# Kernel optimization log

Hardware: AMD Instinct MI355X
Metric: run time of the kernel (lower is better)

## Reference

```python
import jax, jax.numpy as jnp
import numpy as np

R = 2  # decimation factor


def _cheby1_sos(N=8, rp=0.05, Wn=1.0 / R):
    """Chebyshev type-I lowpass, second-order sections (matches scipy.signal.cheby1 math)."""
    eps = np.sqrt(10.0 ** (rp / 10.0) - 1.0)
    mu = np.arcsinh(1.0 / eps) / N
    k = np.arange(1, N + 1)
    theta = np.pi * (2 * k - 1) / (2 * N)
    # analog prototype poles (no zeros)
    p = -np.sinh(mu) * np.sin(theta) + 1j * np.cosh(mu) * np.cos(theta)
    gain = np.real(np.prod(-p))
    if N % 2 == 0:
        gain /= np.sqrt(1.0 + eps * eps)
    # prewarp + lp2lp
    fs = 2.0
    warped = 2.0 * fs * np.tan(np.pi * Wn / fs)
    p = p * warped
    gain = gain * warped ** N
    # bilinear transform (zeros -> z=-1, order N)
    fs2 = 2.0 * fs
    pz = (fs2 + p) / (fs2 - p)
    gain = gain / np.real(np.prod(fs2 - p))
    # pair complex-conjugate poles into biquads (N even, all complex)
    pp = pz[np.imag(pz) > 0]
    a1 = -2.0 * np.real(pp)
    a2 = np.abs(pp) ** 2
    g = gain ** (1.0 / len(pp))  # distribute gain evenly across sections
    b0 = np.full(len(pp), g)
    sos = np.stack([b0, 2.0 * b0, b0, np.ones(len(pp)), a1, a2], axis=1)
    return sos  # [nsec, 6] float64


_SOS = _cheby1_sos()


def _sosfilt(x):
    """Cascaded biquads, direct form II transposed, zero initial state. x: [B, T]."""
    B = x.shape[0]
    nsec = _SOS.shape[0]
    b0 = jnp.asarray(_SOS[:, 0], x.dtype)
    b1 = jnp.asarray(_SOS[:, 1], x.dtype)
    b2 = jnp.asarray(_SOS[:, 2], x.dtype)
    a1 = jnp.asarray(_SOS[:, 4], x.dtype)
    a2 = jnp.asarray(_SOS[:, 5], x.dtype)

    def step(carry, xt):  # carry: (z1, z2) each [B, nsec]; xt: [B]
        z1, z2 = carry
        y = xt
        nz1, nz2 = [], []
        for s in range(nsec):  # fixed small unroll over sections
            out = b0[s] * y + z1[:, s]
            nz1.append(b1[s] * y + z2[:, s] - a1[s] * out)
            nz2.append(b2[s] * y - a2[s] * out)
            y = out
        return (jnp.stack(nz1, axis=1), jnp.stack(nz2, axis=1)), y

    z0 = jnp.zeros((B, nsec), x.dtype)
    _, ys = jax.lax.scan(step, (z0, z0), x.T)  # scan over time
    return ys.T  # [B, T]


def setup_inputs() -> dict:
    key = jax.random.key(0)
    x = jax.random.normal(key, (32, 131072), dtype=jnp.float32)
    return {"x": x}


def reference(x) -> jnp.ndarray:
    y = _sosfilt(x)
    return y[..., ::R]
```

## Files before the change

### kernel.cpp

```cpp
#include <hip/hip_runtime.h>
#include <cmath>
#include <complex>


#define T_LEN   131072
#define B_ROWS  32
#define OUT_LEN (T_LEN / 2)
#define L_CHUNK 64
#define H_WARM  192
#define TPB     256
#define BLOCKS_PER_ROW (T_LEN / (L_CHUNK * TPB))
#define WIN_FLOATS (TPB * L_CHUNK + H_WARM)
#define WIN_UNITS  (WIN_FLOATS / 4)
#define NBLOCKS (B_ROWS * BLOCKS_PER_ROW)

struct Coef { float g; float a1[4]; float a2[4]; };

__global__ __launch_bounds__(256) void cheby_decimate_kernel(
    const float* __restrict__ x, float* __restrict__ out, Coef c)
{
    __shared__ float4 lds[WIN_UNITS];
    const int t   = threadIdx.x;
    const int row = blockIdx.x / BLOCKS_PER_ROW;
    const int bc  = blockIdx.x % BLOCKS_PER_ROW;
    const float* __restrict__ xr = x + (size_t)row * T_LEN;
    const int wstart = bc * (TPB * L_CHUNK) - H_WARM;

    #pragma unroll
    for (int k = 0; k < (WIN_UNITS + TPB - 1) / TPB; ++k) {
        int w = t + TPB * k;
        if (w < WIN_UNITS) {
            int g = wstart + 4 * w;
            float4 v = make_float4(0.f, 0.f, 0.f, 0.f);
            if (g >= 0) v = *reinterpret_cast<const float4*>(xr + g);
            lds[w ^ ((w >> 4) & 7)] = v;
        }
    }
    __syncthreads();

    const float g0   = c.g;
    const float na10 = -c.a1[0], na20 = -c.a2[0];
    const float na11 = -c.a1[1], na21 = -c.a2[1];
    const float na12 = -c.a1[2], na22 = -c.a2[2];
    const float na13 = -c.a1[3], na23 = -c.a2[3];

    float z11=0.f,z12=0.f, z21=0.f,z22=0.f, z31=0.f,z32=0.f, z41=0.f,z42=0.f;

#define LREAD(u) lds[(u) ^ (((u) >> 4) & 7)]
#define STEP(yv) do {                                                          \
        float y = (yv); float w_, o, tt;                                       \
        w_ = g0*y; o = w_ + z11; tt = fmaf(2.f, w_, z12);                      \
        z11 = fmaf(na10, o, tt); z12 = fmaf(na20, o, w_); y = o;               \
        w_ = g0*y; o = w_ + z21; tt = fmaf(2.f, w_, z22);                      \
        z21 = fmaf(na11, o, tt); z22 = fmaf(na21, o, w_); y = o;               \
        w_ = g0*y; o = w_ + z31; tt = fmaf(2.f, w_, z32);                      \
        z31 = fmaf(na12, o, tt); z32 = fmaf(na22, o, w_); y = o;               \
        w_ = g0*y; o = w_ + z41; tt = fmaf(2.f, w_, z42);                      \
        z41 = fmaf(na13, o, tt); z42 = fmaf(na23, o, w_); y = o;               \
        (yv) = y;                                                              \
    } while (0)

    const int ub = 16 * t;
    float4 cur = LREAD(ub);
    float outv[32];

    #pragma unroll 4
    for (int j = 0; j < 48; ++j) {
        float4 nxt = LREAD(ub + j + 1);
        STEP(cur.x); STEP(cur.y); STEP(cur.z); STEP(cur.w);
        cur = nxt;
    }
    #pragma unroll
    for (int j = 48; j < 64; ++j) {
        float4 nxt = (j < 63) ? LREAD(ub + j + 1) : make_float4(0.f,0.f,0.f,0.f);
        STEP(cur.x); STEP(cur.y); STEP(cur.z); STEP(cur.w);
        outv[2*(j-48)]   = cur.x;
        outv[2*(j-48)+1] = cur.z;
        cur = nxt;
    }
#undef STEP
#undef LREAD

    __syncthreads();
    #pragma unroll
    for (int q = 0; q < 8; ++q) {
        lds[8*t + (q ^ (t & 7))] =
            make_float4(outv[4*q], outv[4*q+1], outv[4*q+2], outv[4*q+3]);
    }
    __syncthreads();
    const size_t obase = (size_t)row * OUT_LEN + (size_t)bc * (TPB * L_CHUNK / 2);
    #pragma unroll
    for (int k = 0; k < 8; ++k) {
        int v = t + TPB * k;
        float4 d = lds[(v & ~7) + ((v & 7) ^ ((v >> 3) & 7))];
        *reinterpret_cast<float4*>(out + obase + 4 * v) = d;
    }
}

extern "C" void kernel_launch(void* const* d_in, const int* in_sizes, int n_in,
                              void* d_out, int out_size, void* d_ws, size_t ws_size,
                              hipStream_t stream)
{
    const float* x = (const float*)d_in[0];
    float* out = (float*)d_out;

    const int N = 8;
    const double rp = 0.05;
    const double eps = std::sqrt(std::pow(10.0, rp / 10.0) - 1.0);
    const double mu  = std::asinh(1.0 / eps) / N;

    std::complex<double> p[8];
    std::complex<double> prodnp(1.0, 0.0);
    for (int i = 0; i < N; ++i) {
        double theta = M_PI * (2.0 * (i + 1) - 1.0) / (2.0 * N);
        p[i] = std::complex<double>(-std::sinh(mu) * std::sin(theta),
                                     std::cosh(mu) * std::cos(theta));
        prodnp *= -p[i];
    }
    double gain = prodnp.real() / std::sqrt(1.0 + eps * eps);

    const double fs = 2.0;
    const double warped = 2.0 * fs * std::tan(M_PI * 0.5 / fs);
    std::complex<double> prodden(1.0, 0.0);
    std::complex<double> pz[8];
    for (int i = 0; i < N; ++i) {
        p[i] *= warped;
        pz[i] = (2.0 * fs + p[i]) / (2.0 * fs - p[i]);
        prodden *= (2.0 * fs - p[i]);
    }
    gain *= std::pow(warped, (double)N);
    gain /= prodden.real();

    Coef c;
    int ns = 0;
    double A1[4], A2[4];
    for (int i = 0; i < N; ++i) {
        if (pz[i].imag() > 0.0) {
            A1[ns] = -2.0 * pz[i].real();
            A2[ns] = std::norm(pz[i]);
            ++ns;
        }
    }
    const double gsec = std::pow(gain, 1.0 / ns);
    c.g = (float)gsec;
    for (int s = 0; s < 4; ++s) { c.a1[s] = (float)A1[s]; c.a2[s] = (float)A2[s]; }

    dim3 block(TPB), grid(NBLOCKS);
    hipLaunchKernelGGL(cheby_decimate_kernel, grid, block, 0, stream, x, out, c);
}
```

Baseline: 74.91 us.

## Software-pipeline biquad sections across samples and shrink warmup window

Restructures the per-sample cascade so each of the four biquad sections processes a different, time-skewed sample in each step. The four sections become independent within a step instead of one serial chain, which exposes instruction-level parallelism and shortens the dependency latency per sample. The warmup history is also cut from 192 to 128 samples, reducing redundant filtering work and the load footprint. A few padding LDS units are zeroed to cover the pipeline drain. The shorter warmup may slightly raise truncation error in the filter state at chunk boundaries.

```diff
diff --git a/kernel.cpp b/kernel.cpp
--- a/kernel.cpp
+++ b/kernel.cpp
@@ -7,11 +7,12 @@
 #define B_ROWS  32
 #define OUT_LEN (T_LEN / 2)
 #define L_CHUNK 64
-#define H_WARM  192
+#define H_WARM  128
 #define TPB     256
 #define BLOCKS_PER_ROW (T_LEN / (L_CHUNK * TPB))
 #define WIN_FLOATS (TPB * L_CHUNK + H_WARM)
 #define WIN_UNITS  (WIN_FLOATS / 4)
+#define LDS_UNITS  (WIN_UNITS + 8)
 #define NBLOCKS (B_ROWS * BLOCKS_PER_ROW)
 
 struct Coef { float g; float a1[4]; float a2[4]; };
@@ -19,7 +20,7 @@
 __global__ __launch_bounds__(256) void cheby_decimate_kernel(
     const float* __restrict__ x, float* __restrict__ out, Coef c)
 {
-    __shared__ float4 lds[WIN_UNITS];
+    __shared__ float4 lds[LDS_UNITS];
     const int t   = threadIdx.x;
     const int row = blockIdx.x / BLOCKS_PER_ROW;
     const int bc  = blockIdx.x % BLOCKS_PER_ROW;
@@ -36,6 +37,8 @@
             lds[w ^ ((w >> 4) & 7)] = v;
         }
     }
+    if (t < 8)
+        lds[WIN_UNITS + t] = make_float4(0.f, 0.f, 0.f, 0.f);
     __syncthreads();
 
     const float g0   = c.g;
@@ -45,19 +48,20 @@
     const float na13 = -c.a1[3], na23 = -c.a2[3];
 
     float z11=0.f,z12=0.f, z21=0.f,z22=0.f, z31=0.f,z32=0.f, z41=0.f,z42=0.f;
+    float y1=0.f, y2=0.f, y3=0.f;
 
 #define LREAD(u) lds[(u) ^ (((u) >> 4) & 7)]
-#define STEP(yv) do {                                                          \
-        float y = (yv); float w_, o, tt;                                       \
-        w_ = g0*y; o = w_ + z11; tt = fmaf(2.f, w_, z12);                      \
-        z11 = fmaf(na10, o, tt); z12 = fmaf(na20, o, w_); y = o;               \
-        w_ = g0*y; o = w_ + z21; tt = fmaf(2.f, w_, z22);                      \
-        z21 = fmaf(na11, o, tt); z22 = fmaf(na21, o, w_); y = o;               \
-        w_ = g0*y; o = w_ + z31; tt = fmaf(2.f, w_, z32);                      \
-        z31 = fmaf(na12, o, tt); z32 = fmaf(na22, o, w_); y = o;               \
-        w_ = g0*y; o = w_ + z41; tt = fmaf(2.f, w_, z42);                      \
-        z41 = fmaf(na13, o, tt); z42 = fmaf(na23, o, w_); y = o;               \
-        (yv) = y;                                                              \
+#define SEC(yin, z1, z2, na1, na2, oo) do {                                    \
+        float w_ = g0 * (yin); oo = w_ + z1;                                   \
+        z1 = fmaf(na1, oo, fmaf(2.f, w_, z2)); z2 = fmaf(na2, oo, w_);         \
+    } while (0)
+#define PSTEP(xi, STORE) do {                                                  \
+        float o1, o2, o3, o4;                                                  \
+        SEC((xi), z11, z12, na10, na20, o1);                                   \
+        SEC(y1,   z21, z22, na11, na21, o2);                                   \
+        SEC(y2,   z31, z32, na12, na22, o3);                                   \
+        SEC(y3,   z41, z42, na13, na23, o4);                                   \
+        y1 = o1; y2 = o2; y3 = o3; STORE;                                      \
     } while (0)
 
     const int ub = 16 * t;
@@ -65,20 +69,24 @@
     float outv[32];
 
     #pragma unroll 4
-    for (int j = 0; j < 48; ++j) {
-        float4 nxt = LREAD(ub + j + 1);
-        STEP(cur.x); STEP(cur.y); STEP(cur.z); STEP(cur.w);
+    for (int m = 0; m < 32; ++m) {
+        float4 nxt = LREAD(ub + m + 1);
+        PSTEP(cur.x, (void)0); PSTEP(cur.y, (void)0);
+        PSTEP(cur.z, (void)0); PSTEP(cur.w, (void)0);
         cur = nxt;
     }
     #pragma unroll
-    for (int j = 48; j < 64; ++j) {
-        float4 nxt = (j < 63) ? LREAD(ub + j + 1) : make_float4(0.f,0.f,0.f,0.f);
-        STEP(cur.x); STEP(cur.y); STEP(cur.z); STEP(cur.w);
-        outv[2*(j-48)]   = cur.x;
-        outv[2*(j-48)+1] = cur.z;
+    for (int m = 32; m <= 48; ++m) {
+        float4 nxt = (m < 48) ? LREAD(ub + m + 1)
+                              : make_float4(0.f, 0.f, 0.f, 0.f);
+        PSTEP(cur.x, (void)0);
+        PSTEP(cur.y, if (m >= 33) outv[2*m - 65] = o4);
+        PSTEP(cur.z, (void)0);
+        PSTEP(cur.w, if (m <= 47) outv[2*m - 64] = o4);
         cur = nxt;
     }
-#undef STEP
+#undef PSTEP
+#undef SEC
 #undef LREAD
 
     __syncthreads();
```

Measured after the change: 71.50 us. 4.6% less time.
